# Performance work log

Hardware: AMD Instinct MI355X
Metric: run time of the kernel (lower is better)

## Reference

```python
import jax, jax.numpy as jnp
import numpy as np

C = 343.0      # speed of sound (init kwarg c)
F = 16         # number of frequency channels (len(omega))
H = 128        # MLP hidden width
N = 131072     # collocation points


def _mlp(coords, W1, b1, W2, b2, W3, b3):
    # coords: [..., 3] -> [..., 2F] (first F = real part, last F = imag part)
    h = jnp.tanh(coords @ W1 + b1)
    h = jnp.tanh(h @ W2 + b2)
    return h @ W3 + b3


def setup_inputs() -> dict:
    key = jax.random.key(0)
    ks = jax.random.split(key, 4)
    inputs = jax.random.normal(ks[0], (N, 3), dtype=jnp.float32)
    # omega = 2*pi*f for f = 100..1600 Hz (matches init kwarg list)
    omega = 2.0 * jnp.pi * 100.0 * jnp.arange(1, F + 1, dtype=jnp.float32)
    s_in = 1.0 / np.sqrt(3.0)
    s_h = 1.0 / np.sqrt(float(H))
    W1 = jax.random.normal(ks[1], (3, H), dtype=jnp.float32) * s_in
    b1 = jnp.zeros((H,), dtype=jnp.float32)
    W2 = jax.random.normal(ks[2], (H, H), dtype=jnp.float32) * s_h
    b2 = jnp.zeros((H,), dtype=jnp.float32)
    W3 = jax.random.normal(ks[3], (H, 2 * F), dtype=jnp.float32) * s_h
    b3 = jnp.zeros((2 * F,), dtype=jnp.float32)
    return {"inputs": inputs, "omega": omega, "W1": W1, "b1": b1,
            "W2": W2, "b2": b2, "W3": W3, "b3": b3}


def reference(inputs, omega, W1, b1, W2, b2, W3, b3):
    # Pointwise network R^3 -> R^{2F} (real/imag stacked).
    f = lambda c3: _mlp(c3, W1, b1, W2, b2, W3, b3)

    # u: complex pressure per point per frequency, [N, F]
    out = _mlp(inputs, W1, b1, W2, b2, W3, b3)           # [N, 2F]
    u = out[:, :F] + 1j * out[:, F:]

    # Full spatial Hessian per point via forward-over-reverse AD (fused
    # replacement for the torch per-channel autograd.grad loop).
    hess = jax.vmap(jax.jacfwd(jax.jacrev(f)))(inputs)   # [N, 2F, 3, 3]
    lap_ri = jnp.einsum('nfii->nf', hess)                # diagonal trace = Laplacian
    lap = lap_ri[:, :F] + 1j * lap_ri[:, F:]             # [N, F] complex

    # PDE residual skips channel 0, exactly as the torch loop (i+1 indexing).
    k2 = (omega[1:] / C) ** 2                            # [F-1]
    residual = lap[:, 1:] + k2 * u[:, 1:]                # [N, F-1]

    # mean over channels then over batch == global mean of |residual|^2
    return jnp.mean(jnp.abs(residual) ** 2)
```

## Files before the change

kernel.cpp:

```cpp
#include <hip/hip_runtime.h>
#include <math.h>

#ifndef __has_builtin
#define __has_builtin(x) 0
#endif

#define NPTS   131072
#define FCH    16
#define CSND   343.0f
#define PB     16
#define BLOCK  256
#define GRID   768
#define NBLK   (NPTS / PB)

typedef _Float16 half8 __attribute__((ext_vector_type(8)));
typedef _Float16 half2v __attribute__((ext_vector_type(2)));
typedef float    f32x4 __attribute__((ext_vector_type(4)));

static __device__ __forceinline__ unsigned pack2(float a, float b) {
#if __has_builtin(__builtin_amdgcn_cvt_pkrtz)
  return __builtin_bit_cast(unsigned, __builtin_amdgcn_cvt_pkrtz(a, b));
#else
  half2v v; v[0] = (_Float16)a; v[1] = (_Float16)b;
  return __builtin_bit_cast(unsigned, v);
#endif
}

static __device__ __forceinline__ float mytanh(float x) {
  float ax = fabsf(x);
  float e  = __expf(-2.0f * ax);
  float r  = (1.0f - e) * __builtin_amdgcn_rcpf(1.0f + e);
  return copysignf(r, x);
}


__global__ __launch_bounds__(BLOCK, 3) void helmholtz_kernel(
    const float* __restrict__ x,
    const float* __restrict__ omega,
    const float* __restrict__ W1,
    const float* __restrict__ b1,
    const float* __restrict__ W2,
    const float* __restrict__ b2,
    const float* __restrict__ W3,
    const float* __restrict__ b3,
    float* __restrict__ out)
{
  __shared__ unsigned s_A[80 * 64];
  __shared__ unsigned s_HG[32 * 64];

  const int tid  = threadIdx.x;
  const int w    = tid >> 6;
  const int l    = tid & 63;
  const int col  = l & 15;
  const int quad = l >> 4;

  const int i2 = l;
  const float a0x = W1[2 * i2],     a0y = W1[128 + 2 * i2], a0z = W1[256 + 2 * i2];
  const float a1x = W1[2 * i2 + 1], a1y = W1[129 + 2 * i2], a1z = W1[257 + 2 * i2];
  const float bb0 = b1[2 * i2],     bb1 = b1[2 * i2 + 1];
  const float wsq0 = a0x * a0x + a0y * a0y + a0z * a0z;
  const float wsq1 = a1x * a1x + a1y * a1y + a1z * a1z;

  half8 w2f[2][4];
#pragma unroll
  for (int ntl = 0; ntl < 2; ntl++) {
    const int n = (2 * w + ntl) * 16 + col;
#pragma unroll
    for (int ks = 0; ks < 4; ks++) {
      half8 f;
#pragma unroll
      for (int j = 0; j < 8; j++)
        f[j] = (_Float16)W2[(ks * 32 + (quad << 3) + j) * 128 + n];
      w2f[ntl][ks] = f;
    }
  }
  half8 w3f[4];
  {
    const int n = (w & 1) * 16 + col;
#pragma unroll
    for (int ks = 0; ks < 4; ks++) {
      half8 f;
#pragma unroll
      for (int j = 0; j < 8; j++)
        f[j] = (_Float16)W3[(ks * 32 + (quad << 3) + j) * 32 + n];
      w3f[ks] = f;
    }
  }

  const float b2r0 = b2[2 * w * 16 + col];
  const float b2r1 = b2[(2 * w + 1) * 16 + col];
  float k2v = 0.0f;
  if (col >= 1) {
    float om = omega[col] * (1.0f / CSND);
    k2v = om * om;
  }
  const float b3v = b3[(w & 1) * 16 + col];

  float wsum = 0.0f;

  for (int blk = blockIdx.x; blk < NBLK; blk += gridDim.x) {
    const int pbase = blk * PB;

#pragma unroll
    for (int it = 0; it < 4; it++) {
      int p = w * 4 + it;
      const float* xp = x + (size_t)(pbase + p) * 3;
      float x0 = xp[0], x1 = xp[1], x2 = xp[2];
      float z0 = fmaf(x0, a0x, fmaf(x1, a0y, fmaf(x2, a0z, bb0)));
      float z1 = fmaf(x0, a1x, fmaf(x1, a1y, fmaf(x2, a1z, bb1)));
      float t0 = mytanh(z0), t1 = mytanh(z1);
      float s0 = 1.0f - t0 * t0, s1 = 1.0f - t1 * t1;
      unsigned u_h  = pack2(t0, t1);
      unsigned u_d0 = pack2(s0 * a0x, s1 * a1x);
      unsigned u_d1 = pack2(s0 * a0y, s1 * a1y);
      unsigned u_d2 = pack2(s0 * a0z, s1 * a1z);
      unsigned u_c  = pack2(-2.0f * t0 * s0 * wsq0, -2.0f * t1 * s1 * wsq1);
      int dcol = (((i2 >> 2) ^ p) << 2) + (i2 & 3);
      s_A[(p)      * 64 + dcol] = u_h;
      s_A[(16 + p) * 64 + dcol] = u_d0;
      s_A[(32 + p) * 64 + dcol] = u_d1;
      s_A[(48 + p) * 64 + dcol] = u_d2;
      s_A[(64 + p) * 64 + dcol] = u_c;
    }
    __syncthreads();

    f32x4 acc[5][2];
#pragma unroll
    for (int mt = 0; mt < 5; mt++)
#pragma unroll
      for (int ntl = 0; ntl < 2; ntl++)
        acc[mt][ntl] = (f32x4){0.0f, 0.0f, 0.0f, 0.0f};

#pragma unroll
    for (int mt = 0; mt < 5; mt++) {
      int m = mt * 16 + col;
#pragma unroll
      for (int ks = 0; ks < 4; ks++) {
        int c = (ks * 4 + quad) ^ col;
        half8 af = *(const half8*)&s_A[m * 64 + (c << 2)];
        acc[mt][0] = __builtin_amdgcn_mfma_f32_16x16x32_f16(af, w2f[0][ks], acc[mt][0], 0, 0, 0);
        acc[mt][1] = __builtin_amdgcn_mfma_f32_16x16x32_f16(af, w2f[1][ks], acc[mt][1], 0, 0, 0);
      }
    }

    {
      _Float16* hg = (_Float16*)s_HG;
#pragma unroll
      for (int ntl = 0; ntl < 2; ntl++) {
        int j = (2 * w + ntl) * 16 + col;
        int chunkj = j >> 3;
        float b2v = ntl ? b2r1 : b2r0;
#pragma unroll
        for (int r = 0; r < 4; r++) {
          int p = quad * 4 + r;
          float z2 = acc[0][ntl][r] + b2v;
          float d0 = acc[1][ntl][r], d1 = acc[2][ntl][r], d2 = acc[3][ntl][r];
          float Av = acc[4][ntl][r];
          float t2 = mytanh(z2);
          float s2 = 1.0f - t2 * t2;
          float g  = s2 * (Av - 2.0f * t2 * (d0 * d0 + d1 * d1 + d2 * d2));
          int base = ((chunkj ^ p) << 3) + (j & 7);
          hg[p * 128 + base]        = (_Float16)t2;
          hg[(16 + p) * 128 + base] = (_Float16)g;
        }
      }
    }
    __syncthreads();

    if (w < 2) {
      f32x4 dy = (f32x4){0.0f, 0.0f, 0.0f, 0.0f};
      f32x4 dl = (f32x4){0.0f, 0.0f, 0.0f, 0.0f};
#pragma unroll
      for (int ks = 0; ks < 4; ks++) {
        int ca = (ks * 4 + quad) ^ col;
        half8 afy = *(const half8*)&s_HG[(col)      * 64 + (ca << 2)];
        half8 afl = *(const half8*)&s_HG[(16 + col) * 64 + (ca << 2)];
        dy = __builtin_amdgcn_mfma_f32_16x16x32_f16(afy, w3f[ks], dy, 0, 0, 0);
        dl = __builtin_amdgcn_mfma_f32_16x16x32_f16(afl, w3f[ks], dl, 0, 0, 0);
      }
      if (col >= 1) {
#pragma unroll
        for (int r = 0; r < 4; r++) {
          float yv  = dy[r] + b3v;
          float res = fmaf(k2v, yv, dl[r]);
          wsum += res * res;
        }
      }
    }
  }

#pragma unroll
  for (int off = 32; off > 0; off >>= 1)
    wsum += __shfl_down(wsum, off, 64);
  if (l == 0)
    atomicAdd(out, wsum * (1.0f / ((float)NPTS * (float)(FCH - 1))));
}

extern "C" void kernel_launch(void* const* d_in, const int* in_sizes, int n_in,
                              void* d_out, int out_size, void* d_ws, size_t ws_size,
                              hipStream_t stream) {
  const float* x     = (const float*)d_in[0];
  const float* omega = (const float*)d_in[1];
  const float* W1    = (const float*)d_in[2];
  const float* b1    = (const float*)d_in[3];
  const float* W2    = (const float*)d_in[4];
  const float* b2    = (const float*)d_in[5];
  const float* W3    = (const float*)d_in[6];
  const float* b3    = (const float*)d_in[7];
  float* out = (float*)d_out;

  (void)hipMemsetAsync(out, 0, sizeof(float), stream);
  helmholtz_kernel<<<GRID, BLOCK, 0, stream>>>(x, omega, W1, b1, W2, b2, W3, b3, out);
}
```

Baseline: 129.2 us.

## Double-buffer shared memory to overlap layer-1 with layer-2 MFMA and drop a barrier

Shared buffers for the layer-1 activations and the layer-2 outputs become double-buffered. The next block's first layer is computed into the alternate buffer while the current block runs its MFMAs, which removes one __syncthreads per iteration. Grid size and launch-bounds occupancy drop from 3 to 2 blocks per CU because of the larger LDS footprint and register pressure. With fewer resident waves there is less latency hiding across blocks, so the gain has to come from overlap inside each block.

```diff
diff --git a/kernel.cpp b/kernel.cpp
--- a/kernel.cpp
+++ b/kernel.cpp
@@ -10,7 +10,7 @@
 #define CSND   343.0f
 #define PB     16
 #define BLOCK  256
-#define GRID   768
+#define GRID   512
 #define NBLK   (NPTS / PB)
 
 typedef _Float16 half8 __attribute__((ext_vector_type(8)));
@@ -34,7 +34,7 @@
 }
 
 
-__global__ __launch_bounds__(BLOCK, 3) void helmholtz_kernel(
+__global__ __launch_bounds__(BLOCK, 2) void helmholtz_kernel(
     const float* __restrict__ x,
     const float* __restrict__ omega,
     const float* __restrict__ W1,
@@ -45,8 +45,8 @@
     const float* __restrict__ b3,
     float* __restrict__ out)
 {
-  __shared__ unsigned s_A[80 * 64];
-  __shared__ unsigned s_HG[32 * 64];
+  __shared__ unsigned s_A[2][80 * 64];
+  __shared__ unsigned s_HG[2][32 * 64];
 
   const int tid  = threadIdx.x;
   const int w    = tid >> 6;
@@ -98,9 +98,9 @@
 
   float wsum = 0.0f;
 
-  for (int blk = blockIdx.x; blk < NBLK; blk += gridDim.x) {
+  auto phaseA = [&](int blk, int buf) {
     const int pbase = blk * PB;
-
+    unsigned* sA = s_A[buf];
 #pragma unroll
     for (int it = 0; it < 4; it++) {
       int p = w * 4 + it;
@@ -116,14 +116,23 @@
       unsigned u_d2 = pack2(s0 * a0z, s1 * a1z);
       unsigned u_c  = pack2(-2.0f * t0 * s0 * wsq0, -2.0f * t1 * s1 * wsq1);
       int dcol = (((i2 >> 2) ^ p) << 2) + (i2 & 3);
-      s_A[(p)      * 64 + dcol] = u_h;
-      s_A[(16 + p) * 64 + dcol] = u_d0;
-      s_A[(32 + p) * 64 + dcol] = u_d1;
-      s_A[(48 + p) * 64 + dcol] = u_d2;
-      s_A[(64 + p) * 64 + dcol] = u_c;
-    }
-    __syncthreads();
-
+      sA[(p)      * 64 + dcol] = u_h;
+      sA[(16 + p) * 64 + dcol] = u_d0;
+      sA[(32 + p) * 64 + dcol] = u_d1;
+      sA[(48 + p) * 64 + dcol] = u_d2;
+      sA[(64 + p) * 64 + dcol] = u_c;
+    }
+  };
+
+  phaseA(blockIdx.x, 0);
+  __syncthreads();
+
+  int parity = 0;
+  for (int blk = blockIdx.x; blk < NBLK; blk += gridDim.x, parity ^= 1) {
+    int nblk = blk + (int)gridDim.x;
+    if (nblk < NBLK) phaseA(nblk, parity ^ 1);
+
+    const unsigned* sA = s_A[parity];
     f32x4 acc[5][2];
 #pragma unroll
     for (int mt = 0; mt < 5; mt++)
@@ -137,14 +146,14 @@
 #pragma unroll
       for (int ks = 0; ks < 4; ks++) {
         int c = (ks * 4 + quad) ^ col;
-        half8 af = *(const half8*)&s_A[m * 64 + (c << 2)];
+        half8 af = *(const half8*)&sA[m * 64 + (c << 2)];
         acc[mt][0] = __builtin_amdgcn_mfma_f32_16x16x32_f16(af, w2f[0][ks], acc[mt][0], 0, 0, 0);
         acc[mt][1] = __builtin_amdgcn_mfma_f32_16x16x32_f16(af, w2f[1][ks], acc[mt][1], 0, 0, 0);
       }
     }
 
     {
-      _Float16* hg = (_Float16*)s_HG;
+      _Float16* hg = (_Float16*)s_HG[parity];
 #pragma unroll
       for (int ntl = 0; ntl < 2; ntl++) {
         int j = (2 * w + ntl) * 16 + col;
@@ -168,13 +177,14 @@
     __syncthreads();
 
     if (w < 2) {
+      const unsigned* hgb = s_HG[parity];
       f32x4 dy = (f32x4){0.0f, 0.0f, 0.0f, 0.0f};
       f32x4 dl = (f32x4){0.0f, 0.0f, 0.0f, 0.0f};
 #pragma unroll
       for (int ks = 0; ks < 4; ks++) {
         int ca = (ks * 4 + quad) ^ col;
-        half8 afy = *(const half8*)&s_HG[(col)      * 64 + (ca << 2)];
-        half8 afl = *(const half8*)&s_HG[(16 + col) * 64 + (ca << 2)];
+        half8 afy = *(const half8*)&hgb[(col)      * 64 + (ca << 2)];
+        half8 afl = *(const half8*)&hgb[(16 + col) * 64 + (ca << 2)];
         dy = __builtin_amdgcn_mfma_f32_16x16x32_f16(afy, w3f[ks], dy, 0, 0, 0);
         dl = __builtin_amdgcn_mfma_f32_16x16x32_f16(afl, w3f[ks], dl, 0, 0, 0);
       }
```

After: 123.9 us. 1.04x faster.
